# Optimization experiments

Measured on AMD Instinct MI355X. Metric: run time of the kernel, lower is better.

Reference implementation:

```python
import jax, jax.numpy as jnp
import numpy as np

# Module constants (from init_kwargs)
NB_IN = 4          # num_blocks_in
NB_OUT = 8         # num_blocks_out
BS_IN = 128        # block_size_in (hard-coded in source)
NHID = 4096
BS_OUT = NHID // NB_OUT   # 512, also att_out
TOPK = 4
DK = 64            # d_k = d_v, n_head = 1


def _group_linear(x, w):
    # x: (B, n_blocks, d_in), w: (n_blocks, d_in, d_out) -> (B, n_blocks, d_out)
    return jnp.einsum('bnd,nde->bne', x, w)


def _attend(q, k, v):
    # single-head scaled dot-product attention
    attn = jax.nn.softmax(jnp.einsum('bqd,bkd->bqk', q, k) / jnp.sqrt(jnp.asarray(DK, q.dtype)), axis=-1)
    return jnp.einsum('bqk,bkd->bqd', attn, v), attn


def setup_inputs() -> dict:
    key = jax.random.key(0)
    ks = jax.random.split(key, 20)
    s = 0.02
    d = {
        'inp': jax.random.normal(ks[0], (1024, NB_IN * BS_IN), jnp.float32),
        'hx': jax.random.normal(ks[1], (1024, NHID), jnp.float32),
        'cx': jax.random.normal(ks[2], (1024, NHID), jnp.float32),
        # inp_att (residual=False): GroupLinear q/k/v + fc
        'ia_wq': jax.random.normal(ks[3], (NB_OUT, BS_OUT, DK), jnp.float32) * s,
        'ia_wk': jax.random.normal(ks[4], (NB_IN + 1, BS_IN, DK), jnp.float32) * s,
        'ia_wv': jax.random.normal(ks[5], (NB_IN + 1, BS_IN, DK), jnp.float32) * s,
        'ia_fc_w': jax.random.normal(ks[6], (DK, BS_OUT), jnp.float32) * s,
        'ia_fc_b': jnp.zeros((BS_OUT,), jnp.float32),
        # mha (residual=True, gated)
        'mha_wq': jax.random.normal(ks[7], (NB_OUT, BS_OUT, DK), jnp.float32) * s,
        'mha_wk': jax.random.normal(ks[8], (NB_OUT, BS_OUT, DK), jnp.float32) * s,
        'mha_wv': jax.random.normal(ks[9], (NB_OUT, BS_OUT, DK), jnp.float32) * s,
        'mha_fc_w': jax.random.normal(ks[10], (DK, BS_OUT), jnp.float32) * s,
        'mha_fc_b': jnp.zeros((BS_OUT,), jnp.float32),
        'mha_gate_w': jax.random.normal(ks[11], (DK, BS_OUT), jnp.float32) * s,
        'mha_gate_b': jnp.zeros((BS_OUT,), jnp.float32),
        # block-diagonal LSTM (BlockLSTM after blockify_params): per-block LSTMCell
        'w_ih': jax.random.normal(ks[12], (NB_OUT, BS_OUT, 4 * BS_OUT), jnp.float32) * s,
        'w_hh': jax.random.normal(ks[13], (NB_OUT, BS_OUT, 4 * BS_OUT), jnp.float32) * s,
        'b_ih': jnp.zeros((NB_OUT, 4 * BS_OUT), jnp.float32),
        'b_hh': jnp.zeros((NB_OUT, 4 * BS_OUT), jnp.float32),
    }
    return d


def _forward(inp, hx, cx, ia_wq, ia_wk, ia_wv, ia_fc_w, ia_fc_b,
             mha_wq, mha_wk, mha_wv, mha_fc_w, mha_fc_b, mha_gate_w, mha_gate_b,
             w_ih, w_hh, b_ih, b_hh):
    B = inp.shape[0]
    # --- input attention (inp_att) ---
    x = inp.reshape(B, NB_IN, BS_IN)
    x = jnp.concatenate([x, jnp.zeros_like(x[:, :1])], axis=1)        # append null block -> (B, NB_IN+1, BS_IN)
    hb = hx.reshape(B, NB_OUT, BS_OUT)
    q = _group_linear(hb, ia_wq)                                      # (B, NB_OUT, DK)
    k = _group_linear(x, ia_wk)
    v = _group_linear(x, ia_wv)
    o, iatt = _attend(q, k, v)                                        # o:(B,NB_OUT,DK), iatt:(B,NB_OUT,NB_IN+1)
    inp_use = (o @ ia_fc_w + ia_fc_b).reshape(B, NB_OUT * BS_OUT)     # residual=False path

    # --- top-k block selection mask (detached) ---
    score = iatt[:, :, 0]                                             # (B, NB_OUT)
    thr = jax.lax.top_k(score, TOPK)[0][:, -1]                        # k-th largest per sample
    mask_blk = (score > thr[:, None] - 0.01).astype(hx.dtype)         # (B, NB_OUT)
    mask = jnp.broadcast_to(mask_blk[:, :, None], (B, NB_OUT, BS_OUT)).reshape(B, NHID)
    mask = jax.lax.stop_gradient(mask)

    # --- block-diagonal LSTM update ---
    xb = inp_use.reshape(B, NB_OUT, BS_OUT)
    cb = cx.reshape(B, NB_OUT, BS_OUT)
    gates = (jnp.einsum('bkd,kdg->bkg', xb, w_ih) + b_ih
             + jnp.einsum('bkd,kdg->bkg', hb, w_hh) + b_hh)           # (B, NB_OUT, 4*BS_OUT)
    i_g, f_g, g_g, o_g = jnp.split(gates, 4, axis=-1)
    c_new = jax.nn.sigmoid(f_g) * cb + jax.nn.sigmoid(i_g) * jnp.tanh(g_g)
    h_new = jax.nn.sigmoid(o_g) * jnp.tanh(c_new)                     # (B, NB_OUT, BS_OUT)
    cx_new = c_new.reshape(B, NHID)

    # --- inter-block attention (step_att, residual + gate) ---
    residual = h_new
    q2 = _group_linear(h_new, mha_wq)
    k2 = _group_linear(h_new, mha_wk)
    v2 = _group_linear(h_new, mha_wv)
    o2, _ = _attend(q2, k2, v2)                                       # (B, NB_OUT, DK)
    out = o2 @ mha_fc_w + mha_fc_b
    gate = jax.nn.sigmoid(o2 @ mha_gate_w + mha_gate_b)
    hx_new = (residual + gate * jnp.tanh(out)).reshape(B, NHID)

    # --- masked blend of old / new states ---
    hx_out = mask * hx_new + (1.0 - mask) * hx
    cx_out = mask * cx_new + (1.0 - mask) * cx
    return hx_out, cx_out, mask


def reference(inp, hx, cx, ia_wq, ia_wk, ia_wv, ia_fc_w, ia_fc_b,
              mha_wq, mha_wk, mha_wv, mha_fc_w, mha_fc_b, mha_gate_w, mha_gate_b,
              w_ih, w_hh, b_ih, b_hh):
    return _forward(inp, hx, cx, ia_wq, ia_wk, ia_wv, ia_fc_w, ia_fc_b,
                    mha_wq, mha_wk, mha_wv, mha_fc_w, mha_fc_b, mha_gate_w, mha_gate_b,
                    w_ih, w_hh, b_ih, b_hh)
```

## Files before the change

kernel.cpp:

```cpp
#include <hip/hip_runtime.h>
#include <hip/hip_bf16.h>

#define B_    1024
#define NHID_ 4096
#define NBO   8
#define BSO   512
#define DK_   64

typedef __bf16 bf16;
typedef __bf16 bf16x2 __attribute__((ext_vector_type(2)));
typedef __bf16 bf16x4 __attribute__((ext_vector_type(4)));
typedef __bf16 bf16x8 __attribute__((ext_vector_type(8)));
typedef float  f32x4  __attribute__((ext_vector_type(4)));

__device__ __forceinline__ float sigf(float x){
    float e = __expf(-x);
    return __builtin_amdgcn_rcpf(1.0f + e);
}
__device__ __forceinline__ float ftanh(float x){
    float e = __expf(2.0f*x);
    return 1.0f - 2.0f*__builtin_amdgcn_rcpf(e + 1.0f);
}

__device__ __forceinline__ void gload16(const void* g, void* lds){
    __builtin_amdgcn_global_load_lds((const __attribute__((address_space(1))) unsigned int*)g,
                                     (__attribute__((address_space(3))) unsigned int*)lds,
                                     16, 0, 0);
}

__device__ __forceinline__ void sbar(){
    asm volatile("" ::: "memory");
    __builtin_amdgcn_s_barrier();
    asm volatile("" ::: "memory");
}
#define WAITVM(N) asm volatile("s_waitcnt vmcnt(" #N ")" ::: "memory")

__global__ __launch_bounds__(256) void k_prep(
    const float* __restrict__ w_ih, const float* __restrict__ w_hh,
    const float* __restrict__ hx,
    const float* __restrict__ mha_wq, const float* __restrict__ mha_wk,
    const float* __restrict__ mha_wv, const float* __restrict__ ia_fc_w,
    const float* __restrict__ fc_w, const float* __restrict__ gate_w,
    bf16* __restrict__ wT, bf16* __restrict__ hb16, bf16* __restrict__ wqkvT,
    bf16* __restrict__ iafcT, bf16* __restrict__ fcgT)
{
    int bid = blockIdx.x;
    int t = threadIdx.x;
    if (bid < 4096){
        int c0 = (bid & 31)*64;
        int k0 = ((bid>>5)&7)*64;
        int z  = bid>>8;
        int n = z>>1, which = z&1;
        const float* src = (which ? w_hh : w_ih) + (size_t)n*512*2048;
        __shared__ float tile[64][65];
        #pragma unroll
        for (int it=0; it<4; ++it){
            int idx = t + it*256;
            int r = idx>>4, c4 = (idx&15)*4;
            *(float4*)&tile[r][c4] = *(const float4*)&src[(size_t)(k0+r)*2048 + c0 + c4];
        }
        __syncthreads();
        #pragma unroll
        for (int it=0; it<2; ++it){
            int idx = t + it*256;
            int c = idx>>3, r8 = (idx&7)*8;
            bf16x8 v;
            #pragma unroll
            for (int jj=0;jj<8;++jj) v[jj] = (bf16)tile[r8+jj][c];
            *(bf16x8*)&wT[((size_t)n*2048 + c0 + c)*1024 + which*512 + k0 + r8] = v;
        }
        return;
    }
    int gid = (bid-4096)*256 + t;
    if (gid < 1048576){
        float4 v = ((const float4*)hx)[gid];
        bf16x4 o; o.x=(bf16)v.x; o.y=(bf16)v.y; o.z=(bf16)v.z; o.w=(bf16)v.w;
        *(bf16x4*)&hb16[(size_t)gid*4] = o;
        return;
    }
    int e = gid - 1048576;
    if (e < 786432){
        int col = e >> 9, k = e & 511;
        int n = col / 192, c = col - n*192;
        int p = c >> 6, ee = c & 63;
        const float* s = (p==0) ? mha_wq : ((p==1) ? mha_wk : mha_wv);
        wqkvT[e] = (bf16)s[((size_t)n*512 + k)*64 + ee];
        return;
    }
    e -= 786432;
    if (e < 32768){
        int c = e>>6, k = e&63;
        iafcT[e] = (bf16)ia_fc_w[(size_t)k*512 + c];
        return;
    }
    e -= 32768;
    if (e < 65536){
        int cg = e>>6, k = e&63;
        int ct = cg>>6, j = cg&63;
        const float* s = (j<32) ? fc_w : gate_w;
        int col = ct*32 + (j&31);
        fcgT[e] = (bf16)s[(size_t)k*512 + col];
    }
}

__global__ __launch_bounds__(256) void k_qkv(const float* __restrict__ hx,
                                             const float* __restrict__ inp,
                                             const float* __restrict__ ia_wq,
                                             const float* __restrict__ ia_wk,
                                             const float* __restrict__ ia_wv,
                                             float* __restrict__ qbuf,
                                             float* __restrict__ kbuf,
                                             float* __restrict__ vbuf)
{
    int b0 = blockIdx.x*32, y = blockIdx.y, t = threadIdx.x;
    int tx = t&15, ty = t>>4;
    __shared__ float Af[32][36];
    __shared__ float W1[32][68];
    __shared__ float W2[32][68];
    if (y < 8){
        int n = y;
        float acc[2][4] = {};
        for (int k0=0; k0<512; k0+=32){
            { int row=t>>3, c4=(t&7)*4;
              *(float4*)&Af[row][c4] = *(const float4*)&hx[(size_t)(b0+row)*4096 + n*512 + k0 + c4]; }
            #pragma unroll
            for (int j=0;j<2;++j){
                int id = j*256 + t;
                int kk = id>>4, e4 = (id&15)*4;
                *(float4*)&W1[kk][e4] = *(const float4*)&ia_wq[(size_t)n*32768 + (size_t)(k0+kk)*64 + e4];
            }
            __syncthreads();
            #pragma unroll
            for (int kk4=0; kk4<8; ++kk4){
                float4 a0 = *(float4*)&Af[ty*2  ][kk4*4];
                float4 a1 = *(float4*)&Af[ty*2+1][kk4*4];
                #pragma unroll
                for (int j=0;j<4;++j){
                    float4 wv = *(float4*)&W1[kk4*4+j][tx*4];
                    float s0 = (j==0)?a0.x:((j==1)?a0.y:((j==2)?a0.z:a0.w));
                    float s1 = (j==0)?a1.x:((j==1)?a1.y:((j==2)?a1.z:a1.w));
                    acc[0][0]+=s0*wv.x; acc[0][1]+=s0*wv.y; acc[0][2]+=s0*wv.z; acc[0][3]+=s0*wv.w;
                    acc[1][0]+=s1*wv.x; acc[1][1]+=s1*wv.y; acc[1][2]+=s1*wv.z; acc[1][3]+=s1*wv.w;
                }
            }
            __syncthreads();
        }
        #pragma unroll
        for (int r=0;r<2;++r){
            float4 o; o.x=acc[r][0]; o.y=acc[r][1]; o.z=acc[r][2]; o.w=acc[r][3];
            *(float4*)&qbuf[(size_t)(b0+ty*2+r)*512 + n*64 + tx*4] = o;
        }
    } else {
        int jb = y-8;
        float ak[2][4] = {}, av[2][4] = {};
        for (int k0=0; k0<128; k0+=32){
            { int row=t>>3, c4=(t&7)*4;
              *(float4*)&Af[row][c4] = *(const float4*)&inp[(size_t)(b0+row)*512 + jb*128 + k0 + c4]; }
            #pragma unroll
            for (int j=0;j<2;++j){
                int id = j*256 + t;
                int kk = id>>4, e4 = (id&15)*4;
                *(float4*)&W1[kk][e4] = *(const float4*)&ia_wk[(size_t)jb*8192 + (size_t)(k0+kk)*64 + e4];
                *(float4*)&W2[kk][e4] = *(const float4*)&ia_wv[(size_t)jb*8192 + (size_t)(k0+kk)*64 + e4];
            }
            __syncthreads();
            #pragma unroll
            for (int kk4=0; kk4<8; ++kk4){
                float4 a0 = *(float4*)&Af[ty*2  ][kk4*4];
                float4 a1 = *(float4*)&Af[ty*2+1][kk4*4];
                #pragma unroll
                for (int j=0;j<4;++j){
                    float4 wk = *(float4*)&W1[kk4*4+j][tx*4];
                    float4 wv = *(float4*)&W2[kk4*4+j][tx*4];
                    float s0 = (j==0)?a0.x:((j==1)?a0.y:((j==2)?a0.z:a0.w));
                    float s1 = (j==0)?a1.x:((j==1)?a1.y:((j==2)?a1.z:a1.w));
                    ak[0][0]+=s0*wk.x; ak[0][1]+=s0*wk.y; ak[0][2]+=s0*wk.z; ak[0][3]+=s0*wk.w;
                    ak[1][0]+=s1*wk.x; ak[1][1]+=s1*wk.y; ak[1][2]+=s1*wk.z; ak[1][3]+=s1*wk.w;
                    av[0][0]+=s0*wv.x; av[0][1]+=s0*wv.y; av[0][2]+=s0*wv.z; av[0][3]+=s0*wv.w;
                    av[1][0]+=s1*wv.x; av[1][1]+=s1*wv.y; av[1][2]+=s1*wv.z; av[1][3]+=s1*wv.w;
                }
            }
            __syncthreads();
        }
        #pragma unroll
        for (int r=0;r<2;++r){
            float4 ok; ok.x=ak[r][0]; ok.y=ak[r][1]; ok.z=ak[r][2]; ok.w=ak[r][3];
            float4 ov; ov.x=av[r][0]; ov.y=av[r][1]; ov.z=av[r][2]; ov.w=av[r][3];
            *(float4*)&kbuf[(size_t)(b0+ty*2+r)*256 + jb*64 + tx*4] = ok;
            *(float4*)&vbuf[(size_t)(b0+ty*2+r)*256 + jb*64 + tx*4] = ov;
        }
    }
}

__global__ __launch_bounds__(256) void k_score(const float* __restrict__ qbuf,
                                               const float* __restrict__ kbuf,
                                               const float* __restrict__ vbuf,
                                               bf16* __restrict__ obuf,
                                               float* __restrict__ maskb,
                                               float* __restrict__ mask_out)
{
    int t = threadIdx.x, sb = t>>6, ts = t&63;
    int b = blockIdx.x*4 + sb;
    __shared__ float q_s[4][512];
    __shared__ float k_s[4][256];
    __shared__ float v_s[4][256];
    __shared__ float at_s[4][40];
    __shared__ float sc_s[4][8];
    __shared__ float mb_s[4][8];

    #pragma unroll
    for (int r=0;r<8;++r) q_s[sb][ts+r*64] = qbuf[(size_t)b*512 + ts + r*64];
    #pragma unroll
    for (int r=0;r<4;++r){
        k_s[sb][ts+r*64] = kbuf[(size_t)b*256 + ts + r*64];
        v_s[sb][ts+r*64] = vbuf[(size_t)b*256 + ts + r*64];
    }
    __syncthreads();
    if (ts < 40){
        int n = ts/5, j = ts%5;
        float s = 0.f;
        if (j < 4){
            const float* q = &q_s[sb][n*64];
            const float* k = &k_s[sb][j*64];
            for (int e=0;e<64;++e) s += q[e]*k[e];
            s *= 0.125f;
        }
        at_s[sb][ts] = s;
    }
    __syncthreads();
    if (ts < 8){
        float m = at_s[sb][ts*5];
        for (int j=1;j<5;++j) m = fmaxf(m, at_s[sb][ts*5+j]);
        float ex[5]; float sum=0.f;
        for (int j=0;j<5;++j){ ex[j]=__expf(at_s[sb][ts*5+j]-m); sum+=ex[j]; }
        float inv = 1.f/sum;
        for (int j=0;j<5;++j) at_s[sb][ts*5+j] = ex[j]*inv;
        sc_s[sb][ts] = ex[0]*inv;
    }
    __syncthreads();
    if (ts == 0){
        float s[8];
        for (int nn=0;nn<8;++nn) s[nn] = sc_s[sb][nn];
        for (int ii=1;ii<8;++ii){ float key=s[ii]; int jj=ii-1;
            while(jj>=0 && s[jj]<key){ s[jj+1]=s[jj]; --jj; } s[jj+1]=key; }
        float thr = s[3]-0.01f;
        for (int nn=0;nn<8;++nn) mb_s[sb][nn] = (sc_s[sb][nn] > thr) ? 1.0f : 0.0f;
    }
    __syncthreads();
    #pragma unroll
    for (int r=0;r<8;++r){
        int i = ts + r*64;
        int n = i>>6, e = i&63;
        float s = 0.f;
        #pragma unroll
        for (int j=0;j<4;++j) s += at_s[sb][n*5+j]*v_s[sb][j*64+e];
        obuf[(size_t)b*512 + i] = (bf16)s;
    }
    if (ts < 8) maskb[b*8+ts] = mb_s[sb][ts];
    float4* mo = (float4*)(mask_out + (size_t)b*4096);
    #pragma unroll
    for (int r=0;r<16;++r){
        int i4 = ts + r*64;
        float m = mb_s[sb][i4>>7];
        float4 mv; mv.x=m; mv.y=m; mv.z=m; mv.w=m;
        mo[i4] = mv;
    }
}

__global__ __launch_bounds__(256) void k_fc_ia(const bf16* __restrict__ obuf,
                                               const bf16* __restrict__ iafcT,
                                               const float* __restrict__ ia_fc_b,
                                               bf16* __restrict__ xb16)
{
    int bx = blockIdx.x, by = blockIdx.y;
    int t = threadIdx.x, w = t>>6, l = t&63, quad = l>>4, l16 = l&15;
    int wm = w&1, wd = w>>1;
    __shared__ bf16 A_s[64*72];
    __shared__ bf16 W_s[64*72];
    #pragma unroll
    for (int j=0;j<2;++j){
        int c = t + j*256;
        int row = c>>3, seg = c&7;
        *(bf16x8*)&A_s[row*72 + seg*8] = *(const bf16x8*)&obuf[((size_t)bx*64+row)*64 + seg*8];
        *(bf16x8*)&W_s[row*72 + seg*8] = *(const bf16x8*)&iafcT[((size_t)by*64+row)*64 + seg*8];
    }
    __syncthreads();
    f32x4 zero = {0.f,0.f,0.f,0.f};
    f32x4 acc[2][2] = {{zero,zero},{zero,zero}};
    #pragma unroll
    for (int k0=0;k0<64;k0+=32){
        bf16x8 a[2], bb[2];
        #pragma unroll
        for (int r=0;r<2;++r) a[r] = *(const bf16x8*)&A_s[(wm*32+r*16+l16)*72 + k0 + quad*8];
        #pragma unroll
        for (int c=0;c<2;++c) bb[c] = *(const bf16x8*)&W_s[(wd*32+c*16+l16)*72 + k0 + quad*8];
        #pragma unroll
        for (int r=0;r<2;++r)
            #pragma unroll
            for (int c=0;c<2;++c)
                acc[r][c] = __builtin_amdgcn_mfma_f32_16x16x32_bf16(a[r], bb[c], acc[r][c], 0,0,0);
    }
    #pragma unroll
    for (int c=0;c<2;++c){
        int col = by*64 + wd*32 + c*16 + l16;
        float bias = ia_fc_b[col];
        #pragma unroll
        for (int r=0;r<2;++r)
            #pragma unroll
            for (int v=0;v<4;++v){
                int row = bx*64 + wm*32 + r*16 + quad*4 + v;
                xb16[(size_t)row*512 + col] = (bf16)(acc[r][c][v] + bias);
            }
    }
}

__global__ __launch_bounds__(512,2) void k_lstm(
    const bf16* __restrict__ xb16, const bf16* __restrict__ hb16,
    const bf16* __restrict__ wT, const float* __restrict__ b_ih,
    const float* __restrict__ b_hh, const float* __restrict__ cx,
    const float* __restrict__ maskb,
    float* __restrict__ cx_out, bf16* __restrict__ hn16)
{
    int bid = blockIdx.x;
    int n  = bid & 7;
    int i  = bid >> 3;
    int mt = i & 3, nt = i >> 2;
    int b0 = mt*256, d0 = nt*64;

    int t = threadIdx.x;
    int w = t >> 6, l = t & 63;
    int wr = w >> 2, wc = w & 3;
    int quad = l >> 4, l16 = l & 15;

    __shared__ __align__(16) bf16 lds[4*16384];

    int G0 = t;
    int rowA0 = G0>>2, rowA1 = rowA0 + 128;
    int ksA0 = (G0&3) ^ ((rowA0>>1)&3);
    int ksA1 = (G0&3) ^ ((rowA1>>1)&3);
    const bf16* xbP0 = xb16 + (size_t)(b0+rowA0)*4096 + n*512 + ksA0*8;
    const bf16* hbP0 = hb16 + (size_t)(b0+rowA0)*4096 + n*512 + ksA0*8;
    const bf16* xbP1 = xb16 + (size_t)(b0+rowA1)*4096 + n*512 + ksA1*8;
    const bf16* hbP1 = hb16 + (size_t)(b0+rowA1)*4096 + n*512 + ksA1*8;

    int vc0 = G0>>2, vc1 = vc0 + 128;
    int ksB0 = (G0&3) ^ ((vc0>>1)&3);
    int ksB1 = (G0&3) ^ ((vc1>>1)&3);
    const bf16* wb = wT + (size_t)n*2048*1024;
    const bf16* wP0 = wb + (size_t)((vc0>>6)*512 + d0 + (vc0&63))*1024 + ksB0*8;
    const bf16* wP1 = wb + (size_t)((vc1>>6)*512 + d0 + (vc1&63))*1024 + ksB1*8;

    int offA[8], offB[4];
    #pragma unroll
    for (int m=0;m<8;++m){ int R = wr*128 + m*16 + l16; offA[m] = (R*4 + (quad ^ ((R>>1)&3)))*8; }
    #pragma unroll
    for (int nf=0;nf<4;++nf){ int C = wc*64 + nf*16 + l16; offB[nf] = (C*4 + (quad ^ ((C>>1)&3)))*8; }

    auto stA = [&](int buf, int kt){
        const bf16* s0 = (kt<16 ? xbP0 : hbP0) + (kt&15)*32;
        const bf16* s1 = (kt<16 ? xbP1 : hbP1) + (kt&15)*32;
        bf16* dst = &lds[buf*16384 + w*512];
        gload16(s0, dst);
        gload16(s1, dst + 4096);
    };
    auto stB = [&](int buf, int kt){
        bf16* dst = &lds[buf*16384 + 8192 + w*512];
        gload16(wP0 + kt*32, dst);
        gload16(wP1 + kt*32, dst + 4096);
    };

    f32x4 zero = {0.f,0.f,0.f,0.f};
    f32x4 acc[8][4];
    #pragma unroll
    for (int m=0;m<8;++m)
        #pragma unroll
        for (int nf=0;nf<4;++nf) acc[m][nf] = zero;

    stA(0,0); stB(0,0);
    stA(1,1); stB(1,1);
    WAITVM(4);
    sbar();

    #pragma unroll 2
    for (int kt=0; kt<32; ++kt){
        int buf = kt & 3;
        const bf16* Ab = &lds[buf*16384];
        const bf16* Bb = Ab + 8192;
        bf16x8 av[4], bv[4];

        if (kt < 30) stA((kt+2)&3, kt+2);
        #pragma unroll
        for (int m=0;m<4;++m) av[m] = *(const bf16x8*)&Ab[offA[m]];
        #pragma unroll
        for (int nf=0;nf<4;++nf) bv[nf] = *(const bf16x8*)&Bb[offB[nf]];
        __builtin_amdgcn_s_setprio(1);
        #pragma unroll
        for (int m=0;m<4;++m)
            #pragma unroll
            for (int nf=0;nf<4;++nf)
                acc[m][nf] = __builtin_amdgcn_mfma_f32_16x16x32_bf16(av[m], bv[nf], acc[m][nf], 0,0,0);
        __builtin_amdgcn_s_setprio(0);
        sbar();

        if (kt < 30) stB((kt+2)&3, kt+2);
        #pragma unroll
        for (int m=0;m<4;++m) av[m] = *(const bf16x8*)&Ab[offA[4+m]];
        __builtin_amdgcn_s_setprio(1);
        #pragma unroll
        for (int m=0;m<4;++m)
            #pragma unroll
            for (int nf=0;nf<4;++nf)
                acc[4+m][nf] = __builtin_amdgcn_mfma_f32_16x16x32_bf16(av[m], bv[nf], acc[4+m][nf], 0,0,0);
        __builtin_amdgcn_s_setprio(0);
        if (kt < 30) { WAITVM(4); } else { WAITVM(0); }
        sbar();
    }

    float* gbuf = (float*)lds;
    const int GP = 260;
    int dl_t = t & 63;
    int i_t  = t >> 6;
    int d = d0 + dl_t;
    float bi  = b_ih[n*2048 +        d] + b_hh[n*2048 +        d];
    float bff = b_ih[n*2048 +  512 + d] + b_hh[n*2048 +  512 + d];
    float bg  = b_ih[n*2048 + 1024 + d] + b_hh[n*2048 + 1024 + d];
    float bo  = b_ih[n*2048 + 1536 + d] + b_hh[n*2048 + 1536 + d];

    #pragma unroll
    for (int c=0; c<4; ++c){
        if (wr == (c>>1)){
            #pragma unroll
            for (int mm=0; mm<4; ++mm)
                #pragma unroll
                for (int nf=0; nf<4; ++nf)
                    #pragma unroll
                    for (int v=0; v<4; ++v)
                        gbuf[(mm*16 + quad*4 + v)*GP + wc*64 + nf*16 + l16] = acc[(c&1)*4 + mm][nf][v];
        }
        __syncthreads();
        #pragma unroll
        for (int r=0; r<8; ++r){
            int row_l = i_t*8 + r;
            int row_g = b0 + c*64 + row_l;
            float gi = gbuf[row_l*GP +       dl_t] + bi;
            float gf = gbuf[row_l*GP +  64 + dl_t] + bff;
            float gg = gbuf[row_l*GP + 128 + dl_t] + bg;
            float go = gbuf[row_l*GP + 192 + dl_t] + bo;
            size_t gidx = (size_t)row_g*4096 + n*512 + d;
            float cb = cx[gidx];
            float cn = sigf(gf)*cb + sigf(gi)*ftanh(gg);
            float hn = sigf(go)*ftanh(cn);
            float mk = maskb[row_g*8 + n];
            cx_out[gidx] = (mk != 0.f) ? cn : cb;
            hn16[gidx]   = (bf16)hn;
        }
        __syncthreads();
    }
}

__global__ __launch_bounds__(256) void k_proj64(const bf16* __restrict__ hn16,
                                                const bf16* __restrict__ wqkvT,
                                                float* __restrict__ qkv2)
{
    int b0 = blockIdx.x*64, n = blockIdx.y, ct = blockIdx.z;
    int t = threadIdx.x, w = t>>6, l = t&63, quad = l>>4, l16 = l&15;
    int wm = w&1, wd = w>>1;
    __shared__ bf16 A_s[2][256*8];
    __shared__ bf16 B_s[2][256*8];
    f32x4 zero = {0.f,0.f,0.f,0.f};
    f32x4 acc[2][2] = {{zero,zero},{zero,zero}};
    const bf16* ab = hn16 + (size_t)n*512;
    const bf16* wb = wqkvT + ((size_t)n*192 + ct*64)*512;

    auto stage = [&](int buf, int k0){
        int row = t>>2, ss = t&3;
        int seg = ss ^ ((row>>1)&3);
        gload16(ab + (size_t)(b0+row)*4096 + k0 + seg*8, &A_s[buf][(w*64)*8]);
        gload16(wb + (size_t)row*512      + k0 + seg*8, &B_s[buf][(w*64)*8]);
    };

    stage(0, 0);
    for (int it=0; it<16; ++it){
        __syncthreads();
        if (it < 15) stage((it+1)&1, (it+1)*32);
        int buf = it&1;
        bf16x8 a[2], bb[2];
        #pragma unroll
        for (int r=0;r<2;++r){
            int row = wm*32 + r*16 + l16;
            int slot = row*4 + (quad ^ ((row>>1)&3));
            a[r] = *(const bf16x8*)&A_s[buf][slot*8];
        }
        #pragma unroll
        for (int c=0;c<2;++c){
            int col = wd*32 + c*16 + l16;
            int slot = col*4 + (quad ^ ((col>>1)&3));
            bb[c] = *(const bf16x8*)&B_s[buf][slot*8];
        }
        #pragma unroll
        for (int r=0;r<2;++r)
            #pragma unroll
            for (int c=0;c<2;++c)
                acc[r][c] = __builtin_amdgcn_mfma_f32_16x16x32_bf16(a[r], bb[c], acc[r][c], 0,0,0);
    }
    #pragma unroll
    for (int c=0;c<2;++c){
        int col = ct*64 + wd*32 + c*16 + l16;
        #pragma unroll
        for (int r=0;r<2;++r)
            #pragma unroll
            for (int v=0;v<4;++v){
                int row = b0 + wm*32 + r*16 + quad*4 + v;
                qkv2[(size_t)row*1536 + n*192 + col] = acc[r][c][v];
            }
    }
}

__global__ __launch_bounds__(256) void k_att2(const float* __restrict__ qkv2,
                                              bf16* __restrict__ o2buf)
{
    int t = threadIdx.x, sb = t>>6, ts = t&63;
    int b = blockIdx.x*4 + sb;
    __shared__ float q_s[4][512];
    __shared__ float k_s[4][512];
    __shared__ float v_s[4][512];
    __shared__ float at_s[4][64];
    #pragma unroll
    for (int r=0;r<8;++r){
        int i = ts + r*64;
        int n = i>>6, e = i&63;
        const float* src = qkv2 + (size_t)b*1536 + n*192;
        q_s[sb][i] = src[e];
        k_s[sb][i] = src[64+e];
        v_s[sb][i] = src[128+e];
    }
    __syncthreads();
    {
        int n = ts>>3, j = ts&7;
        float s = 0.f;
        const float* q = &q_s[sb][n*64];
        const float* k = &k_s[sb][j*64];
        for (int e=0;e<64;++e) s += q[e]*k[e];
        at_s[sb][ts] = s*0.125f;
    }
    __syncthreads();
    if (ts < 8){
        float m = at_s[sb][ts*8];
        for (int j=1;j<8;++j) m = fmaxf(m, at_s[sb][ts*8+j]);
        float ex[8]; float sum=0.f;
        for (int j=0;j<8;++j){ ex[j]=__expf(at_s[sb][ts*8+j]-m); sum+=ex[j]; }
        float inv = 1.f/sum;
        for (int j=0;j<8;++j) at_s[sb][ts*8+j] = ex[j]*inv;
    }
    __syncthreads();
    #pragma unroll
    for (int r=0;r<8;++r){
        int i = ts + r*64;
        int n = i>>6, e = i&63;
        float s = 0.f;
        #pragma unroll
        for (int j=0;j<8;++j) s += at_s[sb][n*8+j]*v_s[sb][j*64+e];
        o2buf[(size_t)b*512 + i] = (bf16)s;
    }
}

__global__ __launch_bounds__(256) void k_fcgate(const bf16* __restrict__ o2buf,
                                                const bf16* __restrict__ fcgT,
                                                const float* __restrict__ fc_b,
                                                const float* __restrict__ gate_b,
                                                const bf16* __restrict__ hn16,
                                                const float* __restrict__ hx,
                                                const float* __restrict__ maskb,
                                                float* __restrict__ hx_out)
{
    int bx = blockIdx.x, ct0 = blockIdx.y*2;
    int t = threadIdx.x, w = t>>6, l = t&63, quad = l>>4, l16 = l&15;
    __shared__ bf16 A_s[64*72];
    __shared__ bf16 W_s[2][64*72];
    #pragma unroll
    for (int j=0;j<2;++j){
        int c = t + j*256;
        int row = c>>3, seg = c&7;
        *(bf16x8*)&A_s[row*72 + seg*8] = *(const bf16x8*)&o2buf[((size_t)bx*64+row)*64 + seg*8];
        *(bf16x8*)&W_s[0][row*72 + seg*8] = *(const bf16x8*)&fcgT[((size_t)ct0*64+row)*64 + seg*8];
        *(bf16x8*)&W_s[1][row*72 + seg*8] = *(const bf16x8*)&fcgT[((size_t)(ct0+1)*64+row)*64 + seg*8];
    }
    __syncthreads();
    f32x4 zero = {0.f,0.f,0.f,0.f};
    #pragma unroll
    for (int cc=0; cc<2; ++cc){
        int ct = ct0 + cc;
        f32x4 acc[4] = {zero,zero,zero,zero};
        #pragma unroll
        for (int k0=0;k0<64;k0+=32){
            bf16x8 a = *(const bf16x8*)&A_s[(w*16+l16)*72 + k0 + quad*8];
            #pragma unroll
            for (int c=0;c<4;++c){
                bf16x8 bb = *(const bf16x8*)&W_s[cc][(c*16+l16)*72 + k0 + quad*8];
                acc[c] = __builtin_amdgcn_mfma_f32_16x16x32_bf16(a, bb, acc[c], 0,0,0);
            }
        }
        #pragma unroll
        for (int c=0;c<2;++c){
            int d = ct*32 + c*16 + l16;
            float fb = fc_b[d], gb = gate_b[d];
            #pragma unroll
            for (int v=0;v<4;++v){
                int row = bx*64 + w*16 + quad*4 + v;
                int b = row>>3, n = row&7;
                size_t idx = (size_t)b*4096 + n*512 + d;
                float f = acc[c][v]   + fb;
                float g = acc[c+2][v] + gb;
                float hn = (float)hn16[idx];
                float m = maskb[row];
                hx_out[idx] = (m != 0.f) ? (hn + sigf(g)*ftanh(f)) : hx[idx];
            }
        }
    }
}

extern "C" void kernel_launch(void* const* d_in, const int* in_sizes, int n_in,
                              void* d_out, int out_size, void* d_ws, size_t ws_size,
                              hipStream_t stream)
{
    const float* inp       = (const float*)d_in[0];
    const float* hx        = (const float*)d_in[1];
    const float* cx        = (const float*)d_in[2];
    const float* ia_wq     = (const float*)d_in[3];
    const float* ia_wk     = (const float*)d_in[4];
    const float* ia_wv     = (const float*)d_in[5];
    const float* ia_fc_w   = (const float*)d_in[6];
    const float* ia_fc_b   = (const float*)d_in[7];
    const float* mha_wq    = (const float*)d_in[8];
    const float* mha_wk    = (const float*)d_in[9];
    const float* mha_wv    = (const float*)d_in[10];
    const float* mha_fc_w  = (const float*)d_in[11];
    const float* mha_fc_b  = (const float*)d_in[12];
    const float* mha_gate_w= (const float*)d_in[13];
    const float* mha_gate_b= (const float*)d_in[14];
    const float* w_ih      = (const float*)d_in[15];
    const float* w_hh      = (const float*)d_in[16];
    const float* b_ih      = (const float*)d_in[17];
    const float* b_hh      = (const float*)d_in[18];

    float* hx_out  = (float*)d_out;
    float* cx_out  = hx_out + (size_t)B_*NHID_;
    float* mask_out= cx_out + (size_t)B_*NHID_;

    char* p = (char*)d_ws;
    bf16* wT     = (bf16*)p;               p += (size_t)8*2048*1024*2;
    bf16* hb16   = (bf16*)p;               p += (size_t)B_*NHID_*2;
    bf16* xb16   = (bf16*)p;               p += (size_t)B_*NHID_*2;
    bf16* hn16   = (bf16*)p;               p += (size_t)B_*NHID_*2;
    bf16* wqkvT  = (bf16*)p;               p += (size_t)8*192*512*2;
    bf16* iafcT  = (bf16*)p;               p += (size_t)512*64*2;
    bf16* fcgT   = (bf16*)p;               p += (size_t)1024*64*2;
    float* qbuf  = (float*)p;              p += (size_t)B_*512*4;
    float* kbuf  = (float*)p;              p += (size_t)B_*256*4;
    float* vbuf  = (float*)p;              p += (size_t)B_*256*4;
    bf16* obuf   = (bf16*)p;               p += (size_t)B_*8*64*2;
    bf16* o2buf  = (bf16*)p;               p += (size_t)B_*8*64*2;
    float* qkv2  = (float*)p;              p += (size_t)B_*1536*4;
    float* maskb = (float*)p;              p += (size_t)B_*8*4;

    hipLaunchKernelGGL(k_prep, dim3(11648), dim3(256), 0, stream,
                       w_ih, w_hh, hx, mha_wq, mha_wk, mha_wv, ia_fc_w, mha_fc_w, mha_gate_w,
                       wT, hb16, wqkvT, iafcT, fcgT);
    hipLaunchKernelGGL(k_qkv, dim3(32,12), dim3(256), 0, stream,
                       hx, inp, ia_wq, ia_wk, ia_wv, qbuf, kbuf, vbuf);
    hipLaunchKernelGGL(k_score, dim3(256), dim3(256), 0, stream,
                       qbuf, kbuf, vbuf, obuf, maskb, mask_out);
    hipLaunchKernelGGL(k_fc_ia, dim3(128,8), dim3(256), 0, stream, obuf, iafcT, ia_fc_b, xb16);
    hipLaunchKernelGGL(k_lstm, dim3(256), dim3(512), 0, stream,
                       xb16, hb16, wT, b_ih, b_hh, cx, maskb, cx_out, hn16);
    hipLaunchKernelGGL(k_proj64, dim3(16,8,3), dim3(256), 0, stream, hn16, wqkvT, qkv2);
    hipLaunchKernelGGL(k_att2, dim3(256), dim3(256), 0, stream, qkv2, o2buf);
    hipLaunchKernelGGL(k_fcgate, dim3(128,8), dim3(256), 0, stream,
                       o2buf, fcgT, mha_fc_b, mha_gate_b, hn16, hx, maskb, hx_out);
}
```

Baseline: 285.7 us.

## Retile LSTM GEMM to 128x256 tiles with 256 threads and triple buffering

Changes the block-diagonal LSTM GEMM kernel from 256x256 tiles on 512-thread blocks (256 blocks) to 128x256 tiles on 256-thread blocks (512 blocks). Each wave now covers 64 rows and 128 gate columns. The LDS ring goes from four buffers to three smaller ones, and the weight loads are split across two stages. The aim is better occupancy and more blocks in flight over the CUs. The cost is more redundant weight traffic per output, and the mainloop is no longer unrolled.

After: 288.7 us. About the same (+1.1%).

```diff
diff --git a/kernel.cpp b/kernel.cpp
--- a/kernel.cpp
+++ b/kernel.cpp
@@ -314,7 +314,7 @@
     }
 }
 
-__global__ __launch_bounds__(512,2) void k_lstm(
+__global__ __launch_bounds__(256,2) void k_lstm(
     const bf16* __restrict__ xb16, const bf16* __restrict__ hb16,
     const bf16* __restrict__ wT, const float* __restrict__ b_ih,
     const float* __restrict__ b_hh, const float* __restrict__ cx,
@@ -324,75 +324,84 @@
     int bid = blockIdx.x;
     int n  = bid & 7;
     int i  = bid >> 3;
-    int mt = i & 3, nt = i >> 2;
-    int b0 = mt*256, d0 = nt*64;
+    int mt = i & 7, ct = i >> 3;
+    int b0 = mt*128, d0 = ct*64;
 
     int t = threadIdx.x;
     int w = t >> 6, l = t & 63;
-    int wr = w >> 2, wc = w & 3;
+    int wm = w & 1, wg = w >> 1;
     int quad = l >> 4, l16 = l & 15;
 
-    __shared__ __align__(16) bf16 lds[4*16384];
-
-    int G0 = t;
-    int rowA0 = G0>>2, rowA1 = rowA0 + 128;
-    int ksA0 = (G0&3) ^ ((rowA0>>1)&3);
-    int ksA1 = (G0&3) ^ ((rowA1>>1)&3);
-    const bf16* xbP0 = xb16 + (size_t)(b0+rowA0)*4096 + n*512 + ksA0*8;
-    const bf16* hbP0 = hb16 + (size_t)(b0+rowA0)*4096 + n*512 + ksA0*8;
-    const bf16* xbP1 = xb16 + (size_t)(b0+rowA1)*4096 + n*512 + ksA1*8;
-    const bf16* hbP1 = hb16 + (size_t)(b0+rowA1)*4096 + n*512 + ksA1*8;
-
-    int vc0 = G0>>2, vc1 = vc0 + 128;
-    int ksB0 = (G0&3) ^ ((vc0>>1)&3);
-    int ksB1 = (G0&3) ^ ((vc1>>1)&3);
-    const bf16* wb = wT + (size_t)n*2048*1024;
-    const bf16* wP0 = wb + (size_t)((vc0>>6)*512 + d0 + (vc0&63))*1024 + ksB0*8;
-    const bf16* wP1 = wb + (size_t)((vc1>>6)*512 + d0 + (vc1&63))*1024 + ksB1*8;
-
-    int offA[8], offB[4];
-    #pragma unroll
-    for (int m=0;m<8;++m){ int R = wr*128 + m*16 + l16; offA[m] = (R*4 + (quad ^ ((R>>1)&3)))*8; }
-    #pragma unroll
-    for (int nf=0;nf<4;++nf){ int C = wc*64 + nf*16 + l16; offB[nf] = (C*4 + (quad ^ ((C>>1)&3)))*8; }
+    __shared__ __align__(16) bf16 lds[3*12288];
+
+    int GA0 = (w*2)*64 + l, GA1 = GA0 + 64;
+    int rA0 = GA0>>2,       rA1 = GA1>>2;
+    int kA0 = (GA0&3) ^ ((rA0>>1)&3);
+    int kA1 = (GA1&3) ^ ((rA1>>1)&3);
+    const bf16* xbP0 = xb16 + (size_t)(b0+rA0)*4096 + n*512 + kA0*8;
+    const bf16* xbP1 = xb16 + (size_t)(b0+rA1)*4096 + n*512 + kA1*8;
+    const bf16* hbP0 = hb16 + (size_t)(b0+rA0)*4096 + n*512 + kA0*8;
+    const bf16* hbP1 = hb16 + (size_t)(b0+rA1)*4096 + n*512 + kA1*8;
+
+    const bf16* wbn = wT + (size_t)n*2048*1024;
+    int GB0 = (w*4)*64 + l, GB1 = GB0+64, GB2 = GB0+128, GB3 = GB0+192;
+    int vc0 = GB0>>2, vc1 = GB1>>2, vc2 = GB2>>2, vc3 = GB3>>2;
+    int kB0 = (GB0&3) ^ ((vc0>>1)&3);
+    int kB1 = (GB1&3) ^ ((vc1>>1)&3);
+    int kB2 = (GB2&3) ^ ((vc2>>1)&3);
+    int kB3 = (GB3&3) ^ ((vc3>>1)&3);
+    const bf16* wP0 = wbn + (size_t)((vc0>>6)*512 + d0 + (vc0&63))*1024 + kB0*8;
+    const bf16* wP1 = wbn + (size_t)((vc1>>6)*512 + d0 + (vc1&63))*1024 + kB1*8;
+    const bf16* wP2 = wbn + (size_t)((vc2>>6)*512 + d0 + (vc2&63))*1024 + kB2*8;
+    const bf16* wP3 = wbn + (size_t)((vc3>>6)*512 + d0 + (vc3&63))*1024 + kB3*8;
+
+    int offA[4], offB[8];
+    #pragma unroll
+    for (int m=0;m<4;++m){ int R = wm*64 + m*16 + l16; offA[m] = (R*4 + (quad ^ ((R>>1)&3)))*8; }
+    #pragma unroll
+    for (int nf=0;nf<8;++nf){ int C = wg*128 + nf*16 + l16; offB[nf] = 4096 + (C*4 + (quad ^ ((C>>1)&3)))*8; }
 
     auto stA = [&](int buf, int kt){
         const bf16* s0 = (kt<16 ? xbP0 : hbP0) + (kt&15)*32;
         const bf16* s1 = (kt<16 ? xbP1 : hbP1) + (kt&15)*32;
-        bf16* dst = &lds[buf*16384 + w*512];
+        bf16* dst = &lds[buf*12288 + (w*2)*512];
         gload16(s0, dst);
-        gload16(s1, dst + 4096);
+        gload16(s1, dst + 512);
     };
-    auto stB = [&](int buf, int kt){
-        bf16* dst = &lds[buf*16384 + 8192 + w*512];
-        gload16(wP0 + kt*32, dst);
-        gload16(wP1 + kt*32, dst + 4096);
+    auto stB01 = [&](int buf, int kt){
+        bf16* dst = &lds[buf*12288 + 4096 + (w*4)*512];
+        gload16(wP0 + (size_t)kt*32, dst);
+        gload16(wP1 + (size_t)kt*32, dst + 512);
     };
+    auto stB23 = [&](int buf, int kt){
+        bf16* dst = &lds[buf*12288 + 4096 + (w*4)*512];
+        gload16(wP2 + (size_t)kt*32, dst + 1024);
+        gload16(wP3 + (size_t)kt*32, dst + 1536);
+    };
 
     f32x4 zero = {0.f,0.f,0.f,0.f};
-    f32x4 acc[8][4];
-    #pragma unroll
-    for (int m=0;m<8;++m)
-        #pragma unroll
-        for (int nf=0;nf<4;++nf) acc[m][nf] = zero;
-
-    stA(0,0); stB(0,0);
-    stA(1,1); stB(1,1);
-    WAITVM(4);
+    f32x4 acc[4][8];
+    #pragma unroll
+    for (int m=0;m<4;++m)
+        #pragma unroll
+        for (int nf=0;nf<8;++nf) acc[m][nf] = zero;
+
+    stA(0,0); stB01(0,0); stB23(0,0);
+    stA(1,1); stB01(1,1); stB23(1,1);
+    WAITVM(6);
     sbar();
 
-    #pragma unroll 2
+    int buf = 0, pbuf = 2;
+    #pragma unroll 1
     for (int kt=0; kt<32; ++kt){
-        int buf = kt & 3;
-        const bf16* Ab = &lds[buf*16384];
-        const bf16* Bb = Ab + 8192;
+        const bf16* base = &lds[buf*12288];
         bf16x8 av[4], bv[4];
 
-        if (kt < 30) stA((kt+2)&3, kt+2);
-        #pragma unroll
-        for (int m=0;m<4;++m) av[m] = *(const bf16x8*)&Ab[offA[m]];
-        #pragma unroll
-        for (int nf=0;nf<4;++nf) bv[nf] = *(const bf16x8*)&Bb[offB[nf]];
+        if (kt < 30){ stA(pbuf, kt+2); stB01(pbuf, kt+2); }
+        #pragma unroll
+        for (int m=0;m<4;++m) av[m] = *(const bf16x8*)&base[offA[m]];
+        #pragma unroll
+        for (int nf=0;nf<4;++nf) bv[nf] = *(const bf16x8*)&base[offB[nf]];
         __builtin_amdgcn_s_setprio(1);
         #pragma unroll
         for (int m=0;m<4;++m)
@@ -402,18 +411,19 @@
         __builtin_amdgcn_s_setprio(0);
         sbar();
 
-        if (kt < 30) stB((kt+2)&3, kt+2);
-        #pragma unroll
-        for (int m=0;m<4;++m) av[m] = *(const bf16x8*)&Ab[offA[4+m]];
+        if (kt < 30) stB23(pbuf, kt+2);
+        #pragma unroll
+        for (int nf=0;nf<4;++nf) bv[nf] = *(const bf16x8*)&base[offB[4+nf]];
         __builtin_amdgcn_s_setprio(1);
         #pragma unroll
         for (int m=0;m<4;++m)
             #pragma unroll
             for (int nf=0;nf<4;++nf)
-                acc[4+m][nf] = __builtin_amdgcn_mfma_f32_16x16x32_bf16(av[m], bv[nf], acc[4+m][nf], 0,0,0);
+                acc[m][4+nf] = __builtin_amdgcn_mfma_f32_16x16x32_bf16(av[m], bv[nf], acc[m][4+nf], 0,0,0);
         __builtin_amdgcn_s_setprio(0);
-        if (kt < 30) { WAITVM(4); } else { WAITVM(0); }
+        if (kt < 30) { WAITVM(6); } else { WAITVM(0); }
         sbar();
+        pbuf = buf; buf = (buf==2) ? 0 : buf+1;
     }
 
     float* gbuf = (float*)lds;
@@ -427,20 +437,20 @@
     float bo  = b_ih[n*2048 + 1536 + d] + b_hh[n*2048 + 1536 + d];
 
     #pragma unroll
-    for (int c=0; c<4; ++c){
-        if (wr == (c>>1)){
+    for (int c=0; c<2; ++c){
+        if (wm == c){
             #pragma unroll
             for (int mm=0; mm<4; ++mm)
                 #pragma unroll
-                for (int nf=0; nf<4; ++nf)
+                for (int nf=0; nf<8; ++nf)
                     #pragma unroll
                     for (int v=0; v<4; ++v)
-                        gbuf[(mm*16 + quad*4 + v)*GP + wc*64 + nf*16 + l16] = acc[(c&1)*4 + mm][nf][v];
+                        gbuf[(mm*16 + quad*4 + v)*GP + wg*128 + nf*16 + l16] = acc[mm][nf][v];
         }
         __syncthreads();
         #pragma unroll
-        for (int r=0; r<8; ++r){
-            int row_l = i_t*8 + r;
+        for (int r=0; r<16; ++r){
+            int row_l = i_t*16 + r;
             int row_g = b0 + c*64 + row_l;
             float gi = gbuf[row_l*GP +       dl_t] + bi;
             float gf = gbuf[row_l*GP +  64 + dl_t] + bff;
@@ -671,7 +681,7 @@
     hipLaunchKernelGGL(k_score, dim3(256), dim3(256), 0, stream,
                        qbuf, kbuf, vbuf, obuf, maskb, mask_out);
     hipLaunchKernelGGL(k_fc_ia, dim3(128,8), dim3(256), 0, stream, obuf, iafcT, ia_fc_b, xb16);
-    hipLaunchKernelGGL(k_lstm, dim3(256), dim3(512), 0, stream,
+    hipLaunchKernelGGL(k_lstm, dim3(512), dim3(256), 0, stream,
                        xb16, hb16, wT, b_ih, b_hh, cx, maskb, cx_out, hn16);
     hipLaunchKernelGGL(k_proj64, dim3(16,8,3), dim3(256), 0, stream, hn16, wqkvT, qkv2);
     hipLaunchKernelGGL(k_att2, dim3(256), dim3(256), 0, stream, qkv2, o2buf);
```
